# Performance work log

Measured on AMD Instinct MI355X. Metric: run time of the kernel, lower is better.

The kernel has to match this reference:

```python
import jax, jax.numpy as jnp
import numpy as np

P = 10      # qubits
LQ = 4      # re-uploading layers
B = 4096    # batch
HID = 32    # readout hidden
DIM = 2 ** P


def _rz(t):
    t = jnp.asarray(t, jnp.float32)
    e = jnp.exp(-0.5j * t.astype(jnp.complex64))
    z = jnp.zeros_like(e)
    return jnp.stack([jnp.stack([e, z], -1), jnp.stack([z, jnp.conj(e)], -1)], -2)


def _rx(t):
    t = jnp.asarray(t, jnp.float32)
    c = jnp.cos(0.5 * t).astype(jnp.complex64)
    s = jnp.sin(0.5 * t).astype(jnp.complex64)
    return jnp.stack([jnp.stack([c, -1j * s], -1), jnp.stack([-1j * s, c], -1)], -2)


def _ry(t):
    t = jnp.asarray(t, jnp.float32)
    c = jnp.cos(0.5 * t).astype(jnp.complex64)
    s = jnp.sin(0.5 * t).astype(jnp.complex64)
    return jnp.stack([jnp.stack([c, -s], -1), jnp.stack([s, c], -1)], -2)


def _apply_1q(state, U, k):
    # state [B, 2^P] complex, U [B,2,2]; wire 0 = most-significant bit (PennyLane order)
    b = state.shape[0]
    s = state.reshape(b, 2 ** k, 2, -1)
    s = jnp.einsum('bij,bajc->baic', U, s)
    return s.reshape(b, -1)


def _apply_cnot(state, c, t):
    b = state.shape[0]
    a, d = min(c, t), max(c, t)
    s = state.reshape(b, 2 ** a, 2, 2 ** (d - a - 1), 2, -1)
    if c == a:  # control = smaller wire index (axis 2), target at axis 4
        hi = jnp.flip(s[:, :, 1], axis=3)  # [b,pre,mid,2,post] -> flip target bit
        s = jnp.stack([s[:, :, 0], hi], axis=2)
    else:       # control = larger wire index (axis 4), target at axis 2
        hi = jnp.flip(s[:, :, :, :, 1], axis=2)  # [b,pre,2,mid,post] -> flip target bit
        s = jnp.stack([s[:, :, :, :, 0], hi], axis=4)
    return s.reshape(b, -1)


def _meas_signs(p):
    # rows 0..p-1: Z_k signs; rows p..2p-1: Z_k Z_{(k+1)%p} signs
    idx = np.arange(2 ** p)
    bits = (idx[None, :] >> (p - 1 - np.arange(p)[:, None])) & 1
    z = (1.0 - 2.0 * bits).astype(np.float32)            # [p, 2^p]
    zz = z * np.roll(z, -1, axis=0)                      # [p, 2^p]
    return jnp.asarray(np.concatenate([z, zz], axis=0))  # [2p, 2^p]


MEAS = _meas_signs(P)


def _circuit_feats(theta, rot_weights, enc_scale, enc_bias):
    b = theta.shape[0]
    # Hadamard on every wire of |0...0> -> uniform superposition
    state = jnp.full((b, DIM), 1.0 / np.sqrt(DIM), dtype=jnp.complex64)
    for l in range(LQ):
        for k in range(P):
            t0 = enc_scale[l, k, 0] * theta[:, k] + enc_bias[l, k, 0]
            t1 = enc_scale[l, k, 1] * theta[:, k] + enc_bias[l, k, 1]
            U_enc = jnp.einsum('bij,bjk->bik', _rx(t1), _rz(t0))  # RX(t1) RZ(t0)
            w = rot_weights[l, k]
            # PennyLane Rot(phi,theta,omega) = RZ(omega) RY(theta) RZ(phi)
            U_rot = _rz(w[2]) @ _ry(w[1]) @ _rz(w[0])
            U = jnp.einsum('ij,bjk->bik', U_rot, U_enc)
            state = _apply_1q(state, U, k)
        for k in range(P):
            state = _apply_cnot(state, k, (k + 1) % P)
    probs = jnp.abs(state) ** 2              # [B, 2^P]
    return probs @ MEAS.T                    # [B, 2P] expectation values


def setup_inputs() -> dict:
    key = jax.random.key(0)
    ks = jax.random.split(key, 4)
    theta = jax.random.uniform(ks[0], (B, P), jnp.float32, -np.pi, np.pi)
    rot_weights = 0.02 * jax.random.normal(ks[1], (LQ, P, 3), dtype=jnp.float32)
    enc_scale = jnp.ones((LQ, P, 2), jnp.float32)   # clamp(0.5,1.5) of ones = ones
    enc_bias = jnp.zeros((LQ, P, 2), jnp.float32)
    n_meas = 2 * P
    W1 = jax.random.normal(ks[2], (HID, n_meas), dtype=jnp.float32) / np.sqrt(n_meas)
    b1 = jnp.zeros((HID,), jnp.float32)
    W2 = jax.random.normal(ks[3], (1, HID), dtype=jnp.float32) / np.sqrt(HID)
    b2 = jnp.zeros((1,), jnp.float32)
    return dict(theta=theta, rot_weights=rot_weights, enc_scale=enc_scale,
                enc_bias=enc_bias, W1=W1, b1=b1, W2=W2, b2=b2)


def reference(theta, rot_weights, enc_scale, enc_bias, W1, b1, W2, b2):
    feats = _circuit_feats(theta, rot_weights, enc_scale, enc_bias)
    h = jax.nn.silu(feats @ W1.T + b1)
    return (h @ W2.T + b2)[:, 0]  # [B]
```

## Files before the change

kernel.cpp:

```cpp
#include <hip/hip_runtime.h>
#include <math.h>

#define NQ   10
#define NLAY 4
#define BATCH 4096
#define HID  32
#define NM   20

typedef float    f2  __attribute__((ext_vector_type(2)));
typedef unsigned u2v __attribute__((ext_vector_type(2)));

struct Tables {
    unsigned col[NLAY + 1][NQ];
    unsigned row[NLAY + 1][NQ];
};

constexpr Tables make_tables() {
    Tables t{};
    unsigned col[NQ] = {}, row[NQ] = {};
    for (int k = 0; k < NQ; ++k) { col[k] = 1u << (NQ - 1 - k); row[k] = 1u << (NQ - 1 - k); }
    for (int l = 0; l <= NLAY; ++l) {
        for (int k = 0; k < NQ; ++k) { t.col[l][k] = col[k]; t.row[l][k] = row[k]; }
        for (int k = 0; k < NQ; ++k) {
            int c = k, tg = (k + 1) % NQ;
            col[c] ^= col[tg];
            row[tg] ^= row[c];
        }
    }
    return t;
}

static constexpr Tables TB = make_tables();

struct cpx { float x, y; };
__device__ __forceinline__ cpx cxmul(cpx a, cpx b) {
    return { fmaf(a.x, b.x, -a.y * b.y), fmaf(a.x, b.y, a.y * b.x) };
}

__device__ __forceinline__ f2 mk2(float a, float b) { f2 r; r[0] = a; r[1] = b; return r; }
__device__ __forceinline__ f2 ffma(f2 a, f2 b, f2 c) { return __builtin_elementwise_fma(a, b, c); }

__device__ __forceinline__ f2 cmac(f2 acc, f2 a, f2 b) {
    acc = ffma(mk2(a[0], a[0]), b, acc);
    acc = ffma(mk2(-a[1], a[1]), mk2(b[1], b[0]), acc);
    return acc;
}

template<int CTRL>
__device__ __forceinline__ float dppf(float x) {
    return __int_as_float(__builtin_amdgcn_update_dpp(
        0, __float_as_int(x), CTRL, 0xF, 0xF, true));
}

template<unsigned M>
__device__ __forceinline__ float dpplo(float x) {
    static_assert(M < 16u, "dpplo handles masks 0..15");
    if constexpr (M == 0u)       return x;
    else if constexpr (M == 1u)  return dppf<0xB1>(x);
    else if constexpr (M == 2u)  return dppf<0x4E>(x);
    else if constexpr (M == 3u)  return dppf<0x1B>(x);
    else if constexpr (M == 7u)  return dppf<0x141>(x);
    else if constexpr (M == 8u)  return dppf<0x128>(x);
    else if constexpr (M == 15u) return dppf<0x140>(x);
    else if constexpr (M == 4u)  return dppf<0x141>(dppf<0x1B>(x));
    else if constexpr (M == 5u)  return dppf<0x141>(dppf<0x4E>(x));
    else if constexpr (M == 6u)  return dppf<0x141>(dppf<0xB1>(x));
    else if constexpr (M == 9u)  return dppf<0x128>(dppf<0xB1>(x));
    else if constexpr (M == 10u) return dppf<0x128>(dppf<0x4E>(x));
    else if constexpr (M == 11u) return dppf<0x128>(dppf<0x1B>(x));
    else if constexpr (M == 12u) return dppf<0x140>(dppf<0x1B>(x));
    else if constexpr (M == 13u) return dppf<0x140>(dppf<0x4E>(x));
    else                         return dppf<0x140>(dppf<0xB1>(x));
}

__device__ __forceinline__ float redfold16(float x) {
#if __has_builtin(__builtin_amdgcn_permlane16_swap)
    u2v r = __builtin_amdgcn_permlane16_swap(__float_as_uint(x), __float_as_uint(x), false, false);
    return __uint_as_float(r[0]) + __uint_as_float(r[1]);
#else
    return x + __shfl_xor(x, 16);
#endif
}
__device__ __forceinline__ float redfold32(float x) {
#if __has_builtin(__builtin_amdgcn_permlane32_swap)
    u2v r = __builtin_amdgcn_permlane32_swap(__float_as_uint(x), __float_as_uint(x), false, false);
    return __uint_as_float(r[0]) + __uint_as_float(r[1]);
#else
    return x + __shfl_xor(x, 32);
#endif
}

template<unsigned M>
__device__ __forceinline__ float xlane(float x) {
    if constexpr (M == 0u) return x;
    else if constexpr ((M & 48u) != 0u) return __shfl_xor(x, (int)M);
    else return dpplo<M>(x);
}

template<int L, int K>
__device__ __forceinline__ void apply_gate(f2 (&st)[16],
                                           const float4 (*gm)[2], const int lane) {
    constexpr unsigned v  = TB.col[L][K];
    constexpr unsigned m  = TB.row[L][K];
    constexpr unsigned vl = v >> 4;
    constexpr int      vr = (int)(v & 15u);
    constexpr unsigned ml = m >> 4;
    constexpr int      mr = (int)(m & 15u);
    constexpr int      gi = L * NQ + K;

    int laneP = 0;
    if constexpr (ml != 0) laneP = __popc((unsigned)lane & ml) & 1;
    const float4 A = gm[gi][laneP];
    const f2 ocA = mk2(A.x, A.y), pcA = mk2(A.z, A.w);
    f2 ocB = ocA, pcB = pcA;
    if constexpr (mr != 0) {
        const float4 B = gm[gi][laneP ^ 1];
        ocB = mk2(B.x, B.y); pcB = mk2(B.z, B.w);
    }

    f2 pv[16];
    #pragma unroll
    for (int r = 0; r < 16; ++r) {
        const f2 q = st[r ^ vr];
        if constexpr (vl == 0u) pv[r] = q;
        else pv[r] = mk2(xlane<vl>(q[0]), xlane<vl>(q[1]));
    }
    #pragma unroll
    for (int r = 0; r < 16; ++r) {
        const int pr = __builtin_popcount((unsigned)(r & mr)) & 1;
        const f2 oc = pr ? ocB : ocA;
        const f2 pc = pr ? pcB : pcA;
        f2 acc = mk2(0.f, 0.f);
        acc = cmac(acc, oc, st[r]);
        acc = cmac(acc, pc, pv[r]);
        st[r] = acc;
    }
}

__global__ __launch_bounds__(256, 4) void qrh_kernel(
    const float* __restrict__ theta, const float* __restrict__ rotw,
    const float* __restrict__ escale, const float* __restrict__ ebias,
    const float* __restrict__ W1, const float* __restrict__ b1,
    const float* __restrict__ W2, const float* __restrict__ b2,
    float* __restrict__ out)
{
    __shared__ float4 gmat[4][NLAY * NQ][2];
    __shared__ float4 wtab[4][NQ];

    const int tid  = threadIdx.x;
    const int lane = tid & 63;
    const int wv   = tid >> 6;
    const int b    = blockIdx.x * 4 + wv;

    if (lane < NLAY * NQ) {
        const int g = lane, l = g / NQ, k = g % NQ;
        const float th = theta[b * NQ + k];
        const int e2 = (l * NQ + k) * 2;
        const float t0 = escale[e2 + 0] * th + ebias[e2 + 0];
        const float t1 = escale[e2 + 1] * th + ebias[e2 + 1];
        float sn0, c0, sn1, c1;
        __sincosf(0.5f * t0, &sn0, &c0);
        __sincosf(0.5f * t1, &sn1, &c1);
        const f2 E00 = mk2( c1 * c0,  -c1 * sn0);
        const f2 E01 = mk2( sn1 * sn0, -sn1 * c0);
        const f2 E10 = mk2(-sn1 * sn0, -sn1 * c0);
        const f2 E11 = mk2( c1 * c0,   c1 * sn0);
        const int r3 = (l * NQ + k) * 3;
        const float w0 = rotw[r3 + 0], w1 = rotw[r3 + 1], w2 = rotw[r3 + 2];
        float cw, sw, ca0, sa0, ca1, sa1;
        __sincosf(0.5f * w1, &sw, &cw);
        __sincosf(0.5f * (w0 + w2), &sa0, &ca0);
        __sincosf(0.5f * (w0 - w2), &sa1, &ca1);
        const f2 R00 = mk2( cw * ca0, -cw * sa0);
        const f2 R01 = mk2(-sw * ca1, -sw * sa1);
        const f2 R10 = mk2( sw * ca1, -sw * sa1);
        const f2 R11 = mk2( cw * ca0,  cw * sa0);
        auto cm = [](f2 a, f2 bb) { return mk2(a[0]*bb[0] - a[1]*bb[1], a[0]*bb[1] + a[1]*bb[0]); };
        const f2 U00 = cm(R00, E00) + cm(R01, E10);
        const f2 U01 = cm(R00, E01) + cm(R01, E11);
        const f2 U10 = cm(R10, E00) + cm(R11, E10);
        const f2 U11 = cm(R10, E01) + cm(R11, E11);
        gmat[wv][g][0] = make_float4(U00[0], U00[1], U01[0], U01[1]);
        gmat[wv][g][1] = make_float4(U11[0], U11[1], U10[0], U10[1]);
        if (l == 0) {
            const float inv = 0.70710678118654752f;
            const f2 al = (U00 + U01) * inv;
            const f2 be = (U10 + U11) * inv;
            wtab[wv][k] = make_float4(al[0], al[1], be[0], be[1]);
        }
    }
    __syncthreads();

    f2 st[16];
    {
        cpx pre;
        {
            const float4 q = wtab[wv][0];
            pre = ((lane >> 5) & 1) ? cpx{q.z, q.w} : cpx{q.x, q.y};
            #pragma unroll
            for (int k = 1; k < 6; ++k) {
                const float4 t = wtab[wv][k];
                const cpx w_ = ((lane >> (5 - k)) & 1) ? cpx{t.z, t.w} : cpx{t.x, t.y};
                pre = cxmul(pre, w_);
            }
        }
        const float4 q6 = wtab[wv][6], q7 = wtab[wv][7];
        const float4 q8 = wtab[wv][8], q9 = wtab[wv][9];
        const cpx w6[2] = {{q6.x, q6.y}, {q6.z, q6.w}};
        const cpx w7[2] = {{q7.x, q7.y}, {q7.z, q7.w}};
        const cpx w8[2] = {{q8.x, q8.y}, {q8.z, q8.w}};
        const cpx w9[2] = {{q9.x, q9.y}, {q9.z, q9.w}};
        cpx ph[4], tlo[4];
        #pragma unroll
        for (int a = 0; a < 4; ++a) {
            ph[a]  = cxmul(pre, cxmul(w6[a >> 1], w7[a & 1]));
            tlo[a] = cxmul(w8[a >> 1], w9[a & 1]);
        }
        #pragma unroll
        for (int r = 0; r < 16; ++r) {
            const cpx a0 = cxmul(ph[r >> 2], tlo[r & 3]);
            st[r] = mk2(a0.x, a0.y);
        }
    }

    const float4 (*gm)[2] = gmat[wv];

    #define GATE(L,K) apply_gate<L,K>(st, gm, lane);
    #define LAYER(L) GATE(L,0) GATE(L,1) GATE(L,2) GATE(L,3) GATE(L,4) \
                     GATE(L,5) GATE(L,6) GATE(L,7) GATE(L,8) GATE(L,9)
    LAYER(1)
    LAYER(2)
    LAYER(3)
    #undef LAYER
    #undef GATE

    float w[16];
    #pragma unroll
    for (int r = 0; r < 16; ++r) {
        const f2 sq = st[r] * st[r];
        w[r] = sq[0] + sq[1];
    }
    #pragma unroll
    for (int bit = 1; bit < 16; bit <<= 1) {
        #pragma unroll
        for (int j = 0; j < 16; ++j) {
            if (!(j & bit)) {
                const float a = w[j], c = w[j | bit];
                w[j] = a + c; w[j | bit] = a - c;
            }
        }
    }

    float feats[NM];
    #pragma unroll
    for (int f = 0; f < NM; ++f) {
        const unsigned M = (f < NQ) ? TB.row[NLAY][f]
                                    : (TB.row[NLAY][f - NQ] ^ TB.row[NLAY][(f - NQ + 1) % NQ]);
        const int Ml = (int)(M >> 4), Mj = (int)(M & 15u);
        const float s = w[Mj];
        const int lsgn = __popc((unsigned)lane & (unsigned)Ml) & 1;
        feats[f] = lsgn ? -s : s;
    }
    #pragma unroll
    for (int f = 0; f < NM; ++f) {
        float v = feats[f];
        v += dppf<0xB1>(v);
        v += dppf<0x4E>(v);
        v += dppf<0x141>(v);
        v += dppf<0x128>(v);
        v = redfold16(v);
        v = redfold32(v);
        feats[f] = v;
    }

    float part = 0.f;
    if (lane < HID) {
        float acc = b1[lane];
        #pragma unroll
        for (int mm = 0; mm < NM; ++mm) acc = fmaf(feats[mm], W1[lane * NM + mm], acc);
        const float sg = 1.f / (1.f + __expf(-acc));
        part = acc * sg * W2[lane];
    }
    part += dppf<0xB1>(part);
    part += dppf<0x4E>(part);
    part += dppf<0x141>(part);
    part += dppf<0x128>(part);
    part = redfold16(part);
    part = redfold32(part);
    if (lane == 0) out[b] = part + b2[0];
}

extern "C" void kernel_launch(void* const* d_in, const int* in_sizes, int n_in,
                              void* d_out, int out_size, void* d_ws, size_t ws_size,
                              hipStream_t stream) {
    (void)in_sizes; (void)n_in; (void)out_size; (void)d_ws; (void)ws_size;
    const float* theta = (const float*)d_in[0];
    const float* rotw  = (const float*)d_in[1];
    const float* esc   = (const float*)d_in[2];
    const float* ebi   = (const float*)d_in[3];
    const float* W1    = (const float*)d_in[4];
    const float* b1    = (const float*)d_in[5];
    const float* W2    = (const float*)d_in[6];
    const float* b2    = (const float*)d_in[7];
    float* out = (float*)d_out;

    qrh_kernel<<<BATCH / 4, 256, 0, stream>>>(theta, rotw, esc, ebi, W1, b1, W2, b2, out);
}
```

Measured before the change: 96.87 us.

## Map each batch element to a half-wavefront with 32 amplitudes per lane

Changes the state layout so each 32-lane half of a wavefront simulates one circuit, holding 32 complex amplitudes per lane instead of 16 across a full wave. Bit 5 moves into registers, so that bit no longer needs cross-lane shuffles. Gate application now updates amplitude pairs in place, and all 256 threads cooperatively build the gate tables for 8 batch elements per block. The cost is doubled register pressure (launch bounds drop to 2 waves min) and lower occupancy.

After: 95.41 us. No clear change (-1.5%).

```diff
diff --git a/kernel.cpp b/kernel.cpp
--- a/kernel.cpp
+++ b/kernel.cpp
@@ -81,35 +81,27 @@
     return x + __shfl_xor(x, 16);
 #endif
 }
-__device__ __forceinline__ float redfold32(float x) {
-#if __has_builtin(__builtin_amdgcn_permlane32_swap)
-    u2v r = __builtin_amdgcn_permlane32_swap(__float_as_uint(x), __float_as_uint(x), false, false);
-    return __uint_as_float(r[0]) + __uint_as_float(r[1]);
-#else
-    return x + __shfl_xor(x, 32);
-#endif
-}
 
 template<unsigned M>
 __device__ __forceinline__ float xlane(float x) {
     if constexpr (M == 0u) return x;
-    else if constexpr ((M & 48u) != 0u) return __shfl_xor(x, (int)M);
+    else if constexpr ((M & 16u) != 0u) return __shfl_xor(x, (int)M);
     else return dpplo<M>(x);
 }
 
 template<int L, int K>
-__device__ __forceinline__ void apply_gate(f2 (&st)[16],
-                                           const float4 (*gm)[2], const int lane) {
-    constexpr unsigned v  = TB.col[L][K];
-    constexpr unsigned m  = TB.row[L][K];
-    constexpr unsigned vl = v >> 4;
-    constexpr int      vr = (int)(v & 15u);
-    constexpr unsigned ml = m >> 4;
-    constexpr int      mr = (int)(m & 15u);
-    constexpr int      gi = L * NQ + K;
+__device__ __forceinline__ void apply_gate(f2 (&st)[32], const float4 (*gm)[2],
+                                           const int lane) {
+    constexpr unsigned v     = TB.col[L][K];
+    constexpr unsigned m     = TB.row[L][K];
+    constexpr unsigned vlane = (v >> 5) & 31u;
+    constexpr int      vr    = (int)(v & 31u);
+    constexpr unsigned mlane = (m >> 5) & 31u;
+    constexpr int      mr    = (int)(m & 31u);
+    constexpr int      gi    = L * NQ + K;
 
     int laneP = 0;
-    if constexpr (ml != 0) laneP = __popc((unsigned)lane & ml) & 1;
+    if constexpr (mlane != 0u) laneP = __popc((unsigned)lane & mlane) & 1;
     const float4 A = gm[gi][laneP];
     const f2 ocA = mk2(A.x, A.y), pcA = mk2(A.z, A.w);
     f2 ocB = ocA, pcB = pcA;
@@ -118,43 +110,63 @@
         ocB = mk2(B.x, B.y); pcB = mk2(B.z, B.w);
     }
 
-    f2 pv[16];
-    #pragma unroll
-    for (int r = 0; r < 16; ++r) {
-        const f2 q = st[r ^ vr];
-        if constexpr (vl == 0u) pv[r] = q;
-        else pv[r] = mk2(xlane<vl>(q[0]), xlane<vl>(q[1]));
-    }
-    #pragma unroll
-    for (int r = 0; r < 16; ++r) {
-        const int pr = __builtin_popcount((unsigned)(r & mr)) & 1;
-        const f2 oc = pr ? ocB : ocA;
-        const f2 pc = pr ? pcB : pcA;
-        f2 acc = mk2(0.f, 0.f);
-        acc = cmac(acc, oc, st[r]);
-        acc = cmac(acc, pc, pv[r]);
-        st[r] = acc;
-    }
-}
-
-__global__ __launch_bounds__(256, 4) void qrh_kernel(
+    #pragma unroll
+    for (int r = 0; r < 32; ++r) {
+        const int r2 = r ^ vr;
+        if (r2 < r) continue;
+        f2 p_r, p_r2;
+        if constexpr (vlane != 0u) {
+            p_r = mk2(xlane<vlane>(st[r2][0]), xlane<vlane>(st[r2][1]));
+            if (r2 != r)
+                p_r2 = mk2(xlane<vlane>(st[r][0]), xlane<vlane>(st[r][1]));
+        } else {
+            p_r = st[r2];
+            p_r2 = st[r];
+        }
+        {
+            const int pr = __builtin_popcount((unsigned)(r & mr)) & 1;
+            const f2 oc = pr ? ocB : ocA;
+            const f2 pc = pr ? pcB : pcA;
+            f2 acc = mk2(0.f, 0.f);
+            acc = cmac(acc, oc, st[r]);
+            acc = cmac(acc, pc, p_r);
+            if (r2 != r) {
+                const int pr2 = __builtin_popcount((unsigned)(r2 & mr)) & 1;
+                const f2 oc2 = pr2 ? ocB : ocA;
+                const f2 pc2 = pr2 ? pcB : pcA;
+                f2 acc2 = mk2(0.f, 0.f);
+                acc2 = cmac(acc2, oc2, st[r2]);
+                acc2 = cmac(acc2, pc2, p_r2);
+                st[r2] = acc2;
+            }
+            st[r] = acc;
+        }
+    }
+}
+
+__global__ __launch_bounds__(256, 2)
+void qrh_kernel(
     const float* __restrict__ theta, const float* __restrict__ rotw,
     const float* __restrict__ escale, const float* __restrict__ ebias,
     const float* __restrict__ W1, const float* __restrict__ b1,
     const float* __restrict__ W2, const float* __restrict__ b2,
     float* __restrict__ out)
 {
-    __shared__ float4 gmat[4][NLAY * NQ][2];
-    __shared__ float4 wtab[4][NQ];
+    __shared__ float4 gmat[8 * NLAY * NQ][2];
+    __shared__ float4 wtab[8][NQ];
 
     const int tid  = threadIdx.x;
     const int lane = tid & 63;
     const int wv   = tid >> 6;
-    const int b    = blockIdx.x * 4 + wv;
-
-    if (lane < NLAY * NQ) {
-        const int g = lane, l = g / NQ, k = g % NQ;
-        const float th = theta[b * NQ + k];
+    const int e    = (tid & 255) >> 5 >= 0 ? ((wv << 1) | (lane >> 5)) : 0;
+    const int b    = blockIdx.x * 8 + e;
+
+    for (int g = tid; g < 8 * NLAY * NQ; g += 256) {
+        const int ge = g / (NLAY * NQ);
+        const int gg = g % (NLAY * NQ);
+        const int l = gg / NQ, k = gg % NQ;
+        const int gb = blockIdx.x * 8 + ge;
+        const float th = theta[gb * NQ + k];
         const int e2 = (l * NQ + k) * 2;
         const float t0 = escale[e2 + 0] * th + ebias[e2 + 0];
         const float t1 = escale[e2 + 1] * th + ebias[e2 + 1];
@@ -180,50 +192,50 @@
         const f2 U01 = cm(R00, E01) + cm(R01, E11);
         const f2 U10 = cm(R10, E00) + cm(R11, E10);
         const f2 U11 = cm(R10, E01) + cm(R11, E11);
-        gmat[wv][g][0] = make_float4(U00[0], U00[1], U01[0], U01[1]);
-        gmat[wv][g][1] = make_float4(U11[0], U11[1], U10[0], U10[1]);
+        gmat[g][0] = make_float4(U00[0], U00[1], U01[0], U01[1]);
+        gmat[g][1] = make_float4(U11[0], U11[1], U10[0], U10[1]);
         if (l == 0) {
             const float inv = 0.70710678118654752f;
             const f2 al = (U00 + U01) * inv;
             const f2 be = (U10 + U11) * inv;
-            wtab[wv][k] = make_float4(al[0], al[1], be[0], be[1]);
+            wtab[ge][k] = make_float4(al[0], al[1], be[0], be[1]);
         }
     }
     __syncthreads();
 
-    f2 st[16];
+    const int hl = lane & 31;
+    f2 st[32];
     {
         cpx pre;
         {
-            const float4 q = wtab[wv][0];
-            pre = ((lane >> 5) & 1) ? cpx{q.z, q.w} : cpx{q.x, q.y};
+            const float4 q = wtab[e][0];
+            pre = ((hl >> 4) & 1) ? cpx{q.z, q.w} : cpx{q.x, q.y};
             #pragma unroll
-            for (int k = 1; k < 6; ++k) {
-                const float4 t = wtab[wv][k];
-                const cpx w_ = ((lane >> (5 - k)) & 1) ? cpx{t.z, t.w} : cpx{t.x, t.y};
+            for (int k = 1; k < 5; ++k) {
+                const float4 t = wtab[e][k];
+                const cpx w_ = ((hl >> (4 - k)) & 1) ? cpx{t.z, t.w} : cpx{t.x, t.y};
                 pre = cxmul(pre, w_);
             }
         }
-        const float4 q6 = wtab[wv][6], q7 = wtab[wv][7];
-        const float4 q8 = wtab[wv][8], q9 = wtab[wv][9];
+        const float4 q5 = wtab[e][5], q6 = wtab[e][6], q7 = wtab[e][7];
+        const float4 q8 = wtab[e][8], q9 = wtab[e][9];
+        const cpx w5[2] = {{q5.x, q5.y}, {q5.z, q5.w}};
         const cpx w6[2] = {{q6.x, q6.y}, {q6.z, q6.w}};
         const cpx w7[2] = {{q7.x, q7.y}, {q7.z, q7.w}};
         const cpx w8[2] = {{q8.x, q8.y}, {q8.z, q8.w}};
         const cpx w9[2] = {{q9.x, q9.y}, {q9.z, q9.w}};
-        cpx ph[4], tlo[4];
+        cpx a7[8];
         #pragma unroll
-        for (int a = 0; a < 4; ++a) {
-            ph[a]  = cxmul(pre, cxmul(w6[a >> 1], w7[a & 1]));
-            tlo[a] = cxmul(w8[a >> 1], w9[a & 1]);
-        }
+        for (int j = 0; j < 8; ++j)
+            a7[j] = cxmul(cxmul(cxmul(pre, w5[j >> 2]), w6[(j >> 1) & 1]), w7[j & 1]);
         #pragma unroll
-        for (int r = 0; r < 16; ++r) {
-            const cpx a0 = cxmul(ph[r >> 2], tlo[r & 3]);
-            st[r] = mk2(a0.x, a0.y);
-        }
-    }
-
-    const float4 (*gm)[2] = gmat[wv];
+        for (int r = 0; r < 32; ++r) {
+            const cpx t = cxmul(cxmul(a7[r >> 2], w8[(r >> 1) & 1]), w9[r & 1]);
+            st[r] = mk2(t.x, t.y);
+        }
+    }
+
+    const float4 (*gm)[2] = &gmat[e * NLAY * NQ];
 
     #define GATE(L,K) apply_gate<L,K>(st, gm, lane);
     #define LAYER(L) GATE(L,0) GATE(L,1) GATE(L,2) GATE(L,3) GATE(L,4) \
@@ -234,16 +246,16 @@
     #undef LAYER
     #undef GATE
 
-    float w[16];
-    #pragma unroll
-    for (int r = 0; r < 16; ++r) {
+    float w[32];
+    #pragma unroll
+    for (int r = 0; r < 32; ++r) {
         const f2 sq = st[r] * st[r];
         w[r] = sq[0] + sq[1];
     }
     #pragma unroll
-    for (int bit = 1; bit < 16; bit <<= 1) {
+    for (int bit = 1; bit < 32; bit <<= 1) {
         #pragma unroll
-        for (int j = 0; j < 16; ++j) {
+        for (int j = 0; j < 32; ++j) {
             if (!(j & bit)) {
                 const float a = w[j], c = w[j | bit];
                 w[j] = a + c; w[j | bit] = a - c;
@@ -256,9 +268,10 @@
     for (int f = 0; f < NM; ++f) {
         const unsigned M = (f < NQ) ? TB.row[NLAY][f]
                                     : (TB.row[NLAY][f - NQ] ^ TB.row[NLAY][(f - NQ + 1) % NQ]);
-        const int Ml = (int)(M >> 4), Mj = (int)(M & 15u);
-        const float s = w[Mj];
-        const int lsgn = __popc((unsigned)lane & (unsigned)Ml) & 1;
+        const unsigned Mlane = (M >> 5) & 31u;
+        const int Mr = (int)(M & 31u);
+        const float s = w[Mr];
+        const int lsgn = __popc((unsigned)lane & Mlane) & 1;
         feats[f] = lsgn ? -s : s;
     }
     #pragma unroll
@@ -269,25 +282,23 @@
         v += dppf<0x141>(v);
         v += dppf<0x128>(v);
         v = redfold16(v);
-        v = redfold32(v);
         feats[f] = v;
     }
 
-    float part = 0.f;
-    if (lane < HID) {
-        float acc = b1[lane];
+    float part;
+    {
+        float acc = b1[hl];
         #pragma unroll
-        for (int mm = 0; mm < NM; ++mm) acc = fmaf(feats[mm], W1[lane * NM + mm], acc);
+        for (int mm = 0; mm < NM; ++mm) acc = fmaf(feats[mm], W1[hl * NM + mm], acc);
         const float sg = 1.f / (1.f + __expf(-acc));
-        part = acc * sg * W2[lane];
+        part = acc * sg * W2[hl];
     }
     part += dppf<0xB1>(part);
     part += dppf<0x4E>(part);
     part += dppf<0x141>(part);
     part += dppf<0x128>(part);
     part = redfold16(part);
-    part = redfold32(part);
-    if (lane == 0) out[b] = part + b2[0];
+    if (hl == 0) out[b] = part + b2[0];
 }
 
 extern "C" void kernel_launch(void* const* d_in, const int* in_sizes, int n_in,
@@ -304,5 +315,5 @@
     const float* b2    = (const float*)d_in[7];
     float* out = (float*)d_out;
 
-    qrh_kernel<<<BATCH / 4, 256, 0, stream>>>(theta, rotw, esc, ebi, W1, b1, W2, b2, out);
-}
+    qrh_kernel<<<BATCH / 8, 256, 0, stream>>>(theta, rotw, esc, ebi, W1, b1, W2, b2, out);
+}
```
